# Optimization experiments

Measured on AMD Instinct MI355X. Metric: run time of the kernel, lower is better.

The kernel has to match this reference:

```python
import jax, jax.numpy as jnp
import numpy as np

D_MODEL = 1024
MAX_NUM_LAYERS = 4


def setup_inputs() -> dict:
    key = jax.random.key(0)
    ks = jax.random.split(key, 8)
    S, B, D, L = 1024, 2, D_MODEL, 3
    w = lambda k: (jax.random.normal(k, (D, D), dtype=jnp.float32) * 0.02)
    return {
        "x": jax.random.normal(ks[0], (S, B, D), dtype=jnp.float32),
        "layer_outputs": jax.random.normal(ks[1], (L, S, B, D), dtype=jnp.float32),
        "Wq": w(ks[2]), "bq": jnp.zeros((D,), jnp.float32),
        "Wk": w(ks[3]), "bk": jnp.zeros((D,), jnp.float32),
        "Wv": w(ks[4]), "bv": jnp.zeros((D,), jnp.float32),
        "Wo": w(ks[5]), "bo": jnp.zeros((D,), jnp.float32),
        "layer_weights": jnp.ones((MAX_NUM_LAYERS + 1,), jnp.float32),
        "num_heads": 16,
    }


def reference(x, layer_outputs, Wq, bq, Wk, bk, Wv, bv, Wo, bo, layer_weights, num_heads):
    # x: [S, B, D]; layer_outputs: [L, S, B, D] (stacked prev layer outputs)
    S, B, D = x.shape
    H = num_heads
    hd = D // H
    scale = hd ** -0.5
    # q from x only: [S, B*H, hd] -> [BH, S, hd]
    q = (x @ Wq.T + bq).reshape(S, B * H, hd).transpose(1, 0, 2)
    # k/v from x and all previous layer outputs (shared K/V projections)
    xs = jnp.concatenate([x[None], layer_outputs], axis=0)          # [Lp1, S, B, D]
    Lp1 = xs.shape[0]
    k = (xs @ Wk.T + bk).reshape(Lp1, S, B * H, hd).transpose(0, 2, 1, 3)  # [Lp1, BH, S, hd]
    v = (xs @ Wv.T + bv).reshape(Lp1, S, B * H, hd).transpose(0, 2, 1, 3)
    # per-layer scores, softmax over the key axis (torch dim=-2 of stacked scores)
    scores = jnp.einsum('bqd,lbkd->lbqk', q, k) * scale             # [Lp1, BH, S, S]
    attn = jax.nn.softmax(scores, axis=-1)
    lw = jax.nn.softmax(layer_weights[:Lp1])                        # [Lp1]
    combined = jnp.einsum('l,lbqk,lbkd->bqd', lw, attn, v)          # [BH, S, hd]
    combined = combined.transpose(1, 0, 2).reshape(S, B, D)
    return combined @ Wo.T + bo
```

## Files before the change

### kernel.cpp

```cpp
#include <hip/hip_runtime.h>
#include <hip/hip_bf16.h>
#include <math.h>

#define S_LEN   1024
#define BATCH   2
#define DMODEL  1024
#define NHEADS  16
#define HDIM    64
#define BHEADS  32
#define LP1     4
#define ROWS_PL 2048

typedef __attribute__((ext_vector_type(8)))  short bf16x8;
typedef __attribute__((ext_vector_type(4)))  float f32x4;
typedef __attribute__((ext_vector_type(16))) float f32x16;

__device__ inline ushort bf16_rne(float a) {
    unsigned u = __float_as_uint(a);
    return (ushort)((u + 0x7FFFu + ((u >> 16) & 1u)) >> 16);
}
__device__ inline float bf16_up(ushort h) { return __uint_as_float(((unsigned)h) << 16); }
__device__ inline void split_bf16(float a, ushort &hi, ushort &lo) {
    hi = bf16_rne(a);
    lo = bf16_rne(a - bf16_up(hi));
}
__device__ inline uint pk_bf16(float a, float b) {
    float2 f; f.x = a; f.y = b;
    __hip_bfloat162 h = __float22bfloat162_rn(f);
    return *reinterpret_cast<uint*>(&h);
}
#if __has_builtin(__builtin_amdgcn_exp2f)
__device__ inline float fast_exp2(float x) { return __builtin_amdgcn_exp2f(x); }
#else
__device__ inline float fast_exp2(float x) { return exp2f(x); }
#endif

__device__ inline void glds16(const ushort* g, ushort* l) {
    __builtin_amdgcn_global_load_lds(
        (const __attribute__((address_space(1))) void*)g,
        (__attribute__((address_space(3))) void*)l, 16, 0, 0);
}

#define SCLF 0.18033688011112042f

__global__ __launch_bounds__(256)
void presplit(const float* __restrict__ x, const float* __restrict__ lo,
              const float* __restrict__ Wq, const float* __restrict__ Wk,
              const float* __restrict__ Wv, const float* __restrict__ Wo,
              ushort* __restrict__ XsH, ushort* __restrict__ WH,
              ushort* __restrict__ WL)
{
    const int z = blockIdx.z;
    const float* src; ushort* dh; ushort* dl = nullptr; int n;
    if (z == 0)      { src = x;  dh = XsH;           n = 2097152; }
    else if (z == 1) { src = lo; dh = XsH + 2097152; n = 6291456; }
    else {
        const float* wsrc[4] = { Wq, Wk, Wv, Wo };
        src = wsrc[z - 2];
        dh = WH + (size_t)(z - 2) * 1048576;
        if (z == 2 || z == 5) dl = WL + (size_t)(z - 2) * 1048576;
        n = 1048576;
    }
    const int i = (blockIdx.x * 256 + threadIdx.x) * 8;
    if (i >= n) return;
    float v[8];
    *(float4*)&v[0] = *(const float4*)(src + i);
    *(float4*)&v[4] = *(const float4*)(src + i + 4);
    ushort h[8];
    #pragma unroll
    for (int j = 0; j < 8; ++j) h[j] = bf16_rne(v[j]);
    *(uint4*)(dh + i) = *(uint4*)h;
    if (dl) {
        ushort l[8];
        #pragma unroll
        for (int j = 0; j < 8; ++j) l[j] = bf16_rne(v[j] - bf16_up(h[j]));
        *(uint4*)(dl + i) = *(uint4*)l;
    }
}

template<int MODE>
__global__ __launch_bounds__(256)
void proj_g(const ushort* __restrict__ Abf,
            const ushort* __restrict__ Bhg, const ushort* __restrict__ Blg,
            const float* __restrict__ bias,
            float* __restrict__ outf, ushort* __restrict__ outh,
            ushort* __restrict__ outl)
{
    __shared__ ushort smem[3 * 2048];
    ushort* Ah = smem;
    ushort* Bh = smem + 2048;
    ushort* Bl = smem + 4096;

    const int fid = blockIdx.x;
    const int nt = (fid & 7) * 2 + ((fid >> 3) & 1);
    const int mt = fid >> 4;
    const int m0 = mt * 64, n0 = nt * 64;

    const int t  = threadIdx.x;
    const int wv = t >> 6, lane = t & 63;
    const int quad = lane >> 4, r = lane & 15;
    const int wm = wv & 1, wn = wv >> 1;
    const int mBase = wm * 32, nBase = wn * 32;

    const int lrow = lane >> 2;
    const int lch  = ((lane & 3) ^ (lrow & 3)) * 8;
    const ushort* Asrc  = Abf + (size_t)(m0 + wv * 16 + lrow) * DMODEL + lch;
    const ushort* Bhsrc = Bhg + (size_t)(n0 + wv * 16 + lrow) * DMODEL + lch;
    const ushort* Blsrc = Blg + (size_t)(n0 + wv * 16 + lrow) * DMODEL + lch;
    ushort* lA  = Ah + wv * 512;
    ushort* lBh = Bh + wv * 512;
    ushort* lBl = Bl + wv * 512;

    const int q0x = (quad ^ (r & 3)) << 3;
    f32x4 acc[2][2];
    #pragma unroll
    for (int i = 0; i < 2; ++i)
        #pragma unroll
        for (int j = 0; j < 2; ++j) acc[i][j] = (f32x4){0.f, 0.f, 0.f, 0.f};

    for (int k0 = 0; k0 < DMODEL; k0 += 32) {
        glds16(Asrc + k0, lA);
        glds16(Bhsrc + k0, lBh);
        glds16(Blsrc + k0, lBl);
        __syncthreads();
        bf16x8 fa[2], fbh[2], fbl[2];
        #pragma unroll
        for (int i = 0; i < 2; ++i)
            fa[i] = *(const bf16x8*)&Ah[(mBase + i * 16 + r) * 32 + q0x];
        #pragma unroll
        for (int j = 0; j < 2; ++j) {
            fbh[j] = *(const bf16x8*)&Bh[(nBase + j * 16 + r) * 32 + q0x];
            fbl[j] = *(const bf16x8*)&Bl[(nBase + j * 16 + r) * 32 + q0x];
        }
        #pragma unroll
        for (int i = 0; i < 2; ++i)
            #pragma unroll
            for (int j = 0; j < 2; ++j) {
                acc[i][j] = __builtin_amdgcn_mfma_f32_16x16x32_bf16(fa[i], fbh[j], acc[i][j], 0, 0, 0);
                acc[i][j] = __builtin_amdgcn_mfma_f32_16x16x32_bf16(fa[i], fbl[j], acc[i][j], 0, 0, 0);
            }
        __syncthreads();
    }

    const int cn = lane & 15;
    #pragma unroll
    for (int j = 0; j < 2; ++j) {
        const int n = n0 + nBase + j * 16 + cn;
        const float bv = bias[n];
        #pragma unroll
        for (int i = 0; i < 2; ++i) {
            const int mrow = m0 + mBase + i * 16 + quad * 4;
            #pragma unroll
            for (int g = 0; g < 4; ++g) {
                const int m = mrow + g;
                if (MODE == 1) {
                    outf[(size_t)m * DMODEL + n] = acc[i][j][g] + bv;
                } else {
                    const float val = (acc[i][j][g] + bv) * SCLF;
                    const int s = m >> 1, b = m & 1;
                    const int bh = b * 16 + (n >> 6), e = n & 63;
                    const size_t idx = (((size_t)bh * S_LEN) + s) * HDIM + e;
                    ushort hi, lov; split_bf16(val, hi, lov);
                    outh[idx] = hi; outl[idx] = lov;
                }
            }
        }
    }
}

__global__ __launch_bounds__(256, 4)
void proj_kv(const ushort* __restrict__ XsH,
             const ushort* __restrict__ KWh, const ushort* __restrict__ VWh,
             const float* __restrict__ bk, const float* __restrict__ bv,
             ushort* __restrict__ kout, ushort* __restrict__ vout)
{
    __shared__ ushort smem[10240];
    ushort* Ah = smem;
    ushort* Bp = smem + 2048;

    const int t  = threadIdx.x;
    const int m0 = blockIdx.y * 64, n0 = blockIdx.x * 128;
    const int lyr = m0 >> 11;

    const int wv = t >> 6, lane = t & 63;
    const int quad = lane >> 4, r = lane & 15;
    const int wm = wv & 1, wn = wv >> 1;
    const int mBase = wm * 32, nBase = wn * 64;

    const int lrow = lane >> 2;
    const int lch  = ((lane & 3) ^ (lrow & 3)) * 8;

    const ushort* Asrc = XsH + (size_t)(m0 + wv * 16 + lrow) * DMODEL + lch;
    const ushort* Bw[2] = { KWh, VWh };
    const ushort* Bsrc[2][2];
    #pragma unroll
    for (int p = 0; p < 2; ++p)
        #pragma unroll
        for (int seg = 0; seg < 2; ++seg)
            Bsrc[p][seg] = Bw[p] + (size_t)(n0 + wv * 32 + seg * 16 + lrow) * DMODEL + lch;

    const int q0x = (quad ^ (r & 3)) << 3;

    f32x4 aK[2][4], aV[2][4];
    #pragma unroll
    for (int i = 0; i < 2; ++i)
        #pragma unroll
        for (int j = 0; j < 4; ++j) {
            aK[i][j] = (f32x4){0.f, 0.f, 0.f, 0.f};
            aV[i][j] = (f32x4){0.f, 0.f, 0.f, 0.f};
        }

    for (int k0 = 0; k0 < DMODEL; k0 += 32) {
        glds16(Asrc + k0, Ah + wv * 512);
        #pragma unroll
        for (int p = 0; p < 2; ++p)
            #pragma unroll
            for (int seg = 0; seg < 2; ++seg)
                glds16(Bsrc[p][seg] + k0, Bp + p * 4096 + (wv * 2 + seg) * 512);
        __syncthreads();

        bf16x8 fa[2];
        #pragma unroll
        for (int i = 0; i < 2; ++i)
            fa[i] = *(const bf16x8*)&Ah[(mBase + i * 16 + r) * 32 + q0x];
        #pragma unroll
        for (int j = 0; j < 4; ++j) {
            const int off = (nBase + j * 16 + r) * 32 + q0x;
            const bf16x8 fkh = *(const bf16x8*)&Bp[off];
            const bf16x8 fvh = *(const bf16x8*)&Bp[4096 + off];
            #pragma unroll
            for (int i = 0; i < 2; ++i) {
                aK[i][j] = __builtin_amdgcn_mfma_f32_16x16x32_bf16(fa[i], fkh, aK[i][j], 0, 0, 0);
                aV[i][j] = __builtin_amdgcn_mfma_f32_16x16x32_bf16(fa[i], fvh, aV[i][j], 0, 0, 0);
            }
        }
        __syncthreads();
    }

    const int cn = lane & 15;

    #pragma unroll
    for (int j = 0; j < 4; ++j) {
        const int n = n0 + nBase + j * 16 + cn;
        const float bb = bk[n];
        #pragma unroll
        for (int i = 0; i < 2; ++i) {
            #pragma unroll
            for (int g = 0; g < 4; ++g) {
                const int m = m0 + mBase + i * 16 + quad * 4 + g;
                const int rem = m & 2047, s = rem >> 1, b = rem & 1;
                const int bh = lyr * 32 + b * 16 + (n >> 6);
                kout[(((size_t)bh * S_LEN) + s) * HDIM + (n & 63)] = bf16_rne(aK[i][j][g] + bb);
            }
        }
    }

    ushort* T = smem;
    __syncthreads();
    #pragma unroll
    for (int j = 0; j < 4; ++j) {
        const int nloc = nBase + j * 16 + cn;
        const float bb = bv[n0 + nloc];
        #pragma unroll
        for (int i = 0; i < 2; ++i) {
            #pragma unroll
            for (int g = 0; g < 4; ++g) {
                const int mloc = mBase + i * 16 + quad * 4 + g;
                T[nloc * 66 + mloc] = bf16_rne(aV[i][j][g] + bb);
            }
        }
    }
    __syncthreads();
    {
        const int nloc = t >> 1, bsel = t & 1;
        const int n = n0 + nloc, h = n >> 6, e = n & 63;
        const int s0g = (m0 & 2047) >> 1;
        const int bhI = lyr * 32 + bsel * 16 + h;
        ushort* dst = vout + ((size_t)bhI * HDIM + e) * S_LEN + s0g;
        #pragma unroll
        for (int c = 0; c < 4; ++c) {
            ushort tmp[8];
            #pragma unroll
            for (int j = 0; j < 8; ++j)
                tmp[j] = T[nloc * 66 + 2 * (c * 8 + j) + bsel];
            *(uint4*)(dst + c * 8) = *(uint4*)tmp;
        }
    }
}

__global__ __launch_bounds__(256, 2)
void attn_mfma(const ushort* __restrict__ qhg, const ushort* __restrict__ qlg,
               const ushort* __restrict__ kh, const ushort* __restrict__ vth,
               const float* __restrict__ lwraw, float* __restrict__ part)
{
    __shared__ ushort Pa[8 * 1280];

    const int t    = threadIdx.x;
    const int wv   = t >> 6, lane = t & 63;
    const int half = lane >> 5, lid = lane & 31;

    const int fid  = blockIdx.x;
    const int xcd  = fid & 7, slot = fid >> 3;
    const int pair = xcd * 16 + (slot >> 2);
    const int qt   = slot & 3;
    const int bh   = pair & 31, l = pair >> 5;
    const int qbase = qt * 256 + wv * 64;

    float wl;
    {
        float v[LP1], wm = -3.0e38f;
        #pragma unroll
        for (int i = 0; i < LP1; ++i) { v[i] = lwraw[i]; wm = fmaxf(wm, v[i]); }
        float ws = 0.f;
        #pragma unroll
        for (int i = 0; i < LP1; ++i) { v[i] = __expf(v[i] - wm); ws += v[i]; }
        wl = v[l] / ws;
    }

    bf16x8 qh[2][4], ql[2][4];
    #pragma unroll
    for (int u = 0; u < 2; ++u) {
        const size_t qoff = ((size_t)bh * S_LEN + qbase + u * 32 + lid) * HDIM + half * 8;
        #pragma unroll
        for (int es = 0; es < 4; ++es) {
            qh[u][es] = *(const bf16x8*)(qhg + qoff + es * 16);
            ql[u][es] = *(const bf16x8*)(qlg + qoff + es * 16);
        }
    }

    f32x16 o[2][2];
    #pragma unroll
    for (int u = 0; u < 2; ++u)
        #pragma unroll
        for (int d = 0; d < 2; ++d)
            #pragma unroll
            for (int i = 0; i < 16; ++i) o[u][d][i] = 0.f;
    float ls[2][16];
    #pragma unroll
    for (int u = 0; u < 2; ++u)
        #pragma unroll
        for (int i = 0; i < 16; ++i) ls[u][i] = 0.f;

    const size_t kvo = (size_t)(l * BHEADS + bh) * S_LEN * HDIM;

    for (int kt = 0; kt < 16; ++kt) {
        #pragma unroll
        for (int kc = 0; kc < 2; ++kc) {
            bf16x8 kb[4];
            #pragma unroll
            for (int es = 0; es < 4; ++es)
                kb[es] = *(const bf16x8*)(kh + kvo
                          + (size_t)(kt * 64 + kc * 32 + lid) * HDIM + es * 16 + half * 8);

            f32x16 sa[2];
            #pragma unroll
            for (int u = 0; u < 2; ++u)
                #pragma unroll
                for (int i = 0; i < 16; ++i) sa[u][i] = 0.f;
            #pragma unroll
            for (int es = 0; es < 4; ++es)
                #pragma unroll
                for (int u = 0; u < 2; ++u) {
                    sa[u] = __builtin_amdgcn_mfma_f32_32x32x16_bf16(qh[u][es], kb[es], sa[u], 0, 0, 0);
                    sa[u] = __builtin_amdgcn_mfma_f32_32x32x16_bf16(ql[u][es], kb[es], sa[u], 0, 0, 0);
                }

            bf16x8 vb[2][2];
            #pragma unroll
            for (int ks = 0; ks < 2; ++ks)
                #pragma unroll
                for (int dg = 0; dg < 2; ++dg)
                    vb[ks][dg] = *(const bf16x8*)(vth + kvo
                                  + (size_t)(dg * 32 + lid) * S_LEN
                                  + kt * 64 + kc * 32 + ks * 16 + half * 8);

            #pragma unroll
            for (int u = 0; u < 2; ++u) {
                ushort* base = &Pa[(wv * 2 + u) * 1280];
                #pragma unroll
                for (int rr = 0; rr < 16; rr += 2) {
                    const float p0 = fast_exp2(sa[u][rr]);
                    const float p1 = fast_exp2(sa[u][rr + 1]);
                    ls[u][rr]     += p0;
                    ls[u][rr + 1] += p1;
                    const uint pb = pk_bf16(p0, p1);
                    const int q0 = (rr & 3) + 8 * (rr >> 2) + 4 * half;
                    base[q0 * 40 + lid]       = (ushort)pb;
                    base[(q0 + 1) * 40 + lid] = (ushort)(pb >> 16);
                }
            }

            #pragma unroll
            for (int ks = 0; ks < 2; ++ks)
                #pragma unroll
                for (int u = 0; u < 2; ++u) {
                    const bf16x8 pf = *(const bf16x8*)
                        &Pa[(wv * 2 + u) * 1280 + lid * 40 + ks * 16 + half * 8];
                    #pragma unroll
                    for (int dg = 0; dg < 2; ++dg)
                        o[u][dg] = __builtin_amdgcn_mfma_f32_32x32x16_bf16(pf, vb[ks][dg], o[u][dg], 0, 0, 0);
                }
        }
    }

    #pragma unroll
    for (int u = 0; u < 2; ++u)
        #pragma unroll
        for (int rr = 0; rr < 16; ++rr) {
            float v = ls[u][rr];
            #pragma unroll
            for (int off = 1; off < 32; off <<= 1) v += __shfl_xor(v, off, 32);
            ls[u][rr] = v;
        }

    const int b = bh >> 4, hh = bh & 15;
    float* pbase = part + (size_t)l * (ROWS_PL * DMODEL);
    #pragma unroll
    for (int u = 0; u < 2; ++u)
        #pragma unroll
        for (int rr = 0; rr < 16; ++rr) {
            const int q = qbase + u * 32 + 8 * (rr >> 2) + 4 * half + (rr & 3);
            const float sc = wl / ls[u][rr];
            #pragma unroll
            for (int dg = 0; dg < 2; ++dg) {
                const int d = hh * HDIM + dg * 32 + lid;
                pbase[((size_t)q * BATCH + b) * DMODEL + d] = o[u][dg][rr] * sc;
            }
        }
}

__global__ __launch_bounds__(256)
void sum_y(const float* __restrict__ part, ushort* __restrict__ YH)
{
    const int i = (blockIdx.x * 256 + threadIdx.x) * 8;
    float acc[8];
    #pragma unroll
    for (int c = 0; c < 2; ++c) {
        float4 s = *(const float4*)(part + i + c * 4);
        #pragma unroll
        for (int l = 1; l < LP1; ++l) {
            const float4 p = *(const float4*)(part + (size_t)l * 2097152 + i + c * 4);
            s.x += p.x; s.y += p.y; s.z += p.z; s.w += p.w;
        }
        acc[c * 4 + 0] = s.x; acc[c * 4 + 1] = s.y;
        acc[c * 4 + 2] = s.z; acc[c * 4 + 3] = s.w;
    }
    uint out[4];
    #pragma unroll
    for (int c = 0; c < 4; ++c) out[c] = pk_bf16(acc[c * 2], acc[c * 2 + 1]);
    *(uint4*)(YH + i) = *(uint4*)out;
}

extern "C" void kernel_launch(void* const* d_in, const int* in_sizes, int n_in,
                              void* d_out, int out_size, void* d_ws, size_t ws_size,
                              hipStream_t stream) {
    const float* x  = (const float*)d_in[0];
    const float* lo = (const float*)d_in[1];
    const float* Wq = (const float*)d_in[2];
    const float* bq = (const float*)d_in[3];
    const float* Wk = (const float*)d_in[4];
    const float* bk = (const float*)d_in[5];
    const float* Wv = (const float*)d_in[6];
    const float* bv = (const float*)d_in[7];
    const float* Wo = (const float*)d_in[8];
    const float* bo = (const float*)d_in[9];
    const float* lw = (const float*)d_in[10];
    float* out = (float*)d_out;

    char* ws = (char*)d_ws;
    ushort* XsH  = (ushort*)(ws);
    ushort* WH   = (ushort*)(ws + 16777216);
    ushort* WL   = (ushort*)(ws + 25165824);
    ushort* qhb  = (ushort*)(ws + 33554432);
    ushort* qlb  = (ushort*)(ws + 37748736);
    ushort* khb  = (ushort*)(ws + 41943040);
    ushort* vthb = (ushort*)(ws + 58720256);
    float*  part = (float*)(ws + 75497472);
    ushort* YH   = (ushort*)(ws + 109051904);

    dim3 blk(256);
    presplit<<<dim3(3072, 1, 6), blk, 0, stream>>>(x, lo, Wq, Wk, Wv, Wo, XsH, WH, WL);
    proj_g<0><<<dim3(512), blk, 0, stream>>>(XsH, WH, WL, bq, nullptr, qhb, qlb);
    proj_kv<<<dim3(8, 128), blk, 0, stream>>>(XsH,
        WH + 1048576, WH + 2097152, bk, bv, khb, vthb);
    attn_mfma<<<dim3(512), blk, 0, stream>>>(qhb, qlb, khb, vthb, lw, part);
    sum_y<<<dim3(1024), blk, 0, stream>>>(part, YH);
    proj_g<1><<<dim3(512), blk, 0, stream>>>(YH, WH + 3145728, WL + 3145728, bo, out, nullptr, nullptr);
}
```

Measured before the change: 276.0 us.

## Transpose attention MFMA operands and pass P through permlane swap instead of LDS

The attention kernel now computes S^T = K·Q^T so each lane holds one query's scores. The P fragment for the PV MFMA is built in registers with v_permlane32_swap, which removes the LDS staging buffer and its stores and loads. Each wave now handles 32 queries instead of 64, the grid doubles to 1024 blocks, and launch bounds rise to 4 blocks per SIMD for more occupancy. The row-sum reduction collapses to a single cross-half shuffle, and output stores become float4. In exchange, K and V fragments are reused across half as many queries, so global/L2 load traffic per FLOP doubles.

```diff
diff --git a/kernel.cpp b/kernel.cpp
--- a/kernel.cpp
+++ b/kernel.cpp
@@ -34,6 +34,10 @@
 #else
 __device__ inline float fast_exp2(float x) { return exp2f(x); }
 #endif
+
+__device__ inline void permswap(uint &a, uint &b) {
+    asm("v_permlane32_swap_b32 %0, %1" : "+v"(a), "+v"(b));
+}
 
 __device__ inline void glds16(const ushort* g, ushort* l) {
     __builtin_amdgcn_global_load_lds(
@@ -288,23 +292,21 @@
     }
 }
 
-__global__ __launch_bounds__(256, 2)
+__global__ __launch_bounds__(256, 4)
 void attn_mfma(const ushort* __restrict__ qhg, const ushort* __restrict__ qlg,
                const ushort* __restrict__ kh, const ushort* __restrict__ vth,
                const float* __restrict__ lwraw, float* __restrict__ part)
 {
-    __shared__ ushort Pa[8 * 1280];
-
     const int t    = threadIdx.x;
     const int wv   = t >> 6, lane = t & 63;
     const int half = lane >> 5, lid = lane & 31;
 
     const int fid  = blockIdx.x;
     const int xcd  = fid & 7, slot = fid >> 3;
-    const int pair = xcd * 16 + (slot >> 2);
-    const int qt   = slot & 3;
+    const int pair = xcd * 16 + (slot >> 3);
+    const int qt   = slot & 7;
     const int bh   = pair & 31, l = pair >> 5;
-    const int qbase = qt * 256 + wv * 64;
+    const int qbase = qt * 128 + wv * 32;
 
     float wl;
     {
@@ -317,115 +319,87 @@
         wl = v[l] / ws;
     }
 
-    bf16x8 qh[2][4], ql[2][4];
-    #pragma unroll
-    for (int u = 0; u < 2; ++u) {
-        const size_t qoff = ((size_t)bh * S_LEN + qbase + u * 32 + lid) * HDIM + half * 8;
+    bf16x8 qh[4], ql[4];
+    {
+        const size_t qoff = ((size_t)bh * S_LEN + qbase + lid) * HDIM + half * 8;
         #pragma unroll
         for (int es = 0; es < 4; ++es) {
-            qh[u][es] = *(const bf16x8*)(qhg + qoff + es * 16);
-            ql[u][es] = *(const bf16x8*)(qlg + qoff + es * 16);
-        }
-    }
-
-    f32x16 o[2][2];
-    #pragma unroll
-    for (int u = 0; u < 2; ++u)
-        #pragma unroll
-        for (int d = 0; d < 2; ++d)
-            #pragma unroll
-            for (int i = 0; i < 16; ++i) o[u][d][i] = 0.f;
-    float ls[2][16];
-    #pragma unroll
-    for (int u = 0; u < 2; ++u)
-        #pragma unroll
-        for (int i = 0; i < 16; ++i) ls[u][i] = 0.f;
+            qh[es] = *(const bf16x8*)(qhg + qoff + es * 16);
+            ql[es] = *(const bf16x8*)(qlg + qoff + es * 16);
+        }
+    }
+
+    f32x16 o[2];
+    #pragma unroll
+    for (int dg = 0; dg < 2; ++dg)
+        #pragma unroll
+        for (int i = 0; i < 16; ++i) o[dg][i] = 0.f;
+    float ls = 0.f;
 
     const size_t kvo = (size_t)(l * BHEADS + bh) * S_LEN * HDIM;
 
-    for (int kt = 0; kt < 16; ++kt) {
-        #pragma unroll
-        for (int kc = 0; kc < 2; ++kc) {
-            bf16x8 kb[4];
-            #pragma unroll
-            for (int es = 0; es < 4; ++es)
-                kb[es] = *(const bf16x8*)(kh + kvo
-                          + (size_t)(kt * 64 + kc * 32 + lid) * HDIM + es * 16 + half * 8);
-
-            f32x16 sa[2];
-            #pragma unroll
-            for (int u = 0; u < 2; ++u)
-                #pragma unroll
-                for (int i = 0; i < 16; ++i) sa[u][i] = 0.f;
-            #pragma unroll
-            for (int es = 0; es < 4; ++es)
-                #pragma unroll
-                for (int u = 0; u < 2; ++u) {
-                    sa[u] = __builtin_amdgcn_mfma_f32_32x32x16_bf16(qh[u][es], kb[es], sa[u], 0, 0, 0);
-                    sa[u] = __builtin_amdgcn_mfma_f32_32x32x16_bf16(ql[u][es], kb[es], sa[u], 0, 0, 0);
-                }
-
-            bf16x8 vb[2][2];
-            #pragma unroll
-            for (int ks = 0; ks < 2; ++ks)
-                #pragma unroll
-                for (int dg = 0; dg < 2; ++dg)
-                    vb[ks][dg] = *(const bf16x8*)(vth + kvo
-                                  + (size_t)(dg * 32 + lid) * S_LEN
-                                  + kt * 64 + kc * 32 + ks * 16 + half * 8);
-
-            #pragma unroll
-            for (int u = 0; u < 2; ++u) {
-                ushort* base = &Pa[(wv * 2 + u) * 1280];
-                #pragma unroll
-                for (int rr = 0; rr < 16; rr += 2) {
-                    const float p0 = fast_exp2(sa[u][rr]);
-                    const float p1 = fast_exp2(sa[u][rr + 1]);
-                    ls[u][rr]     += p0;
-                    ls[u][rr + 1] += p1;
-                    const uint pb = pk_bf16(p0, p1);
-                    const int q0 = (rr & 3) + 8 * (rr >> 2) + 4 * half;
-                    base[q0 * 40 + lid]       = (ushort)pb;
-                    base[(q0 + 1) * 40 + lid] = (ushort)(pb >> 16);
-                }
-            }
-
-            #pragma unroll
-            for (int ks = 0; ks < 2; ++ks)
-                #pragma unroll
-                for (int u = 0; u < 2; ++u) {
-                    const bf16x8 pf = *(const bf16x8*)
-                        &Pa[(wv * 2 + u) * 1280 + lid * 40 + ks * 16 + half * 8];
-                    #pragma unroll
-                    for (int dg = 0; dg < 2; ++dg)
-                        o[u][dg] = __builtin_amdgcn_mfma_f32_32x32x16_bf16(pf, vb[ks][dg], o[u][dg], 0, 0, 0);
-                }
-        }
-    }
-
-    #pragma unroll
-    for (int u = 0; u < 2; ++u)
-        #pragma unroll
-        for (int rr = 0; rr < 16; ++rr) {
-            float v = ls[u][rr];
-            #pragma unroll
-            for (int off = 1; off < 32; off <<= 1) v += __shfl_xor(v, off, 32);
-            ls[u][rr] = v;
-        }
-
+    for (int kt = 0; kt < 32; ++kt) {
+        const ushort* kp = kh + kvo + (size_t)(kt * 32 + lid) * HDIM + half * 8;
+        bf16x8 kb[4];
+        #pragma unroll
+        for (int es = 0; es < 4; ++es) kb[es] = *(const bf16x8*)(kp + es * 16);
+
+        f32x16 sa;
+        #pragma unroll
+        for (int i = 0; i < 16; ++i) sa[i] = 0.f;
+        #pragma unroll
+        for (int es = 0; es < 4; ++es) {
+            sa = __builtin_amdgcn_mfma_f32_32x32x16_bf16(kb[es], qh[es], sa, 0, 0, 0);
+            sa = __builtin_amdgcn_mfma_f32_32x32x16_bf16(kb[es], ql[es], sa, 0, 0, 0);
+        }
+
+        const ushort* vp = vth + kvo + (size_t)lid * S_LEN + kt * 32 + half * 8;
+        #pragma unroll
+        for (int ks = 0; ks < 2; ++ks) {
+            const float p0 = fast_exp2(sa[8 * ks + 0]);
+            const float p1 = fast_exp2(sa[8 * ks + 1]);
+            const float p2 = fast_exp2(sa[8 * ks + 2]);
+            const float p3 = fast_exp2(sa[8 * ks + 3]);
+            const float p4 = fast_exp2(sa[8 * ks + 4]);
+            const float p5 = fast_exp2(sa[8 * ks + 5]);
+            const float p6 = fast_exp2(sa[8 * ks + 6]);
+            const float p7 = fast_exp2(sa[8 * ks + 7]);
+            ls += ((p0 + p1) + (p2 + p3)) + ((p4 + p5) + (p6 + p7));
+
+            uint a0 = pk_bf16(p0, p1);
+            uint a1 = pk_bf16(p2, p3);
+            uint b0 = pk_bf16(p4, p5);
+            uint b1 = pk_bf16(p6, p7);
+            permswap(a0, b0);
+            permswap(a1, b1);
+            union { uint w[4]; bf16x8 v; } pu;
+            pu.w[0] = a0; pu.w[1] = a1; pu.w[2] = b0; pu.w[3] = b1;
+            const bf16x8 pf = pu.v;
+
+            #pragma unroll
+            for (int dg = 0; dg < 2; ++dg) {
+                const bf16x8 vbf = *(const bf16x8*)(vp + (size_t)dg * (32 * S_LEN) + ks * 16);
+                o[dg] = __builtin_amdgcn_mfma_f32_32x32x16_bf16(vbf, pf, o[dg], 0, 0, 0);
+            }
+        }
+    }
+
+    ls += __shfl_xor(ls, 32);
+    const float sc = wl / ls;
     const int b = bh >> 4, hh = bh & 15;
-    float* pbase = part + (size_t)l * (ROWS_PL * DMODEL);
-    #pragma unroll
-    for (int u = 0; u < 2; ++u)
-        #pragma unroll
-        for (int rr = 0; rr < 16; ++rr) {
-            const int q = qbase + u * 32 + 8 * (rr >> 2) + 4 * half + (rr & 3);
-            const float sc = wl / ls[u][rr];
-            #pragma unroll
-            for (int dg = 0; dg < 2; ++dg) {
-                const int d = hh * HDIM + dg * 32 + lid;
-                pbase[((size_t)q * BATCH + b) * DMODEL + d] = o[u][dg][rr] * sc;
-            }
+    const int q = qbase + lid;
+    float* pb = part + (size_t)l * (ROWS_PL * DMODEL)
+              + ((size_t)q * BATCH + b) * DMODEL + hh * HDIM;
+    #pragma unroll
+    for (int dg = 0; dg < 2; ++dg)
+        #pragma unroll
+        for (int rq = 0; rq < 4; ++rq) {
+            float4 vv;
+            vv.x = o[dg][rq * 4 + 0] * sc;
+            vv.y = o[dg][rq * 4 + 1] * sc;
+            vv.z = o[dg][rq * 4 + 2] * sc;
+            vv.w = o[dg][rq * 4 + 3] * sc;
+            *(float4*)(pb + dg * 32 + rq * 8 + half * 4) = vv;
         }
 }
 
@@ -483,7 +457,7 @@
     proj_g<0><<<dim3(512), blk, 0, stream>>>(XsH, WH, WL, bq, nullptr, qhb, qlb);
     proj_kv<<<dim3(8, 128), blk, 0, stream>>>(XsH,
         WH + 1048576, WH + 2097152, bk, bv, khb, vthb);
-    attn_mfma<<<dim3(512), blk, 0, stream>>>(qhb, qlb, khb, vthb, lw, part);
+    attn_mfma<<<dim3(1024), blk, 0, stream>>>(qhb, qlb, khb, vthb, lw, part);
     sum_y<<<dim3(1024), blk, 0, stream>>>(part, YH);
     proj_g<1><<<dim3(512), blk, 0, stream>>>(YH, WH + 3145728, WL + 3145728, bo, out, nullptr, nullptr);
 }
```

Measured after the change: 328.5 us. 19.0% more time.

## Transpose attention MFMAs to keep softmax probabilities in registers via permlane swap

Applied to the files above, without the earlier changes.

The attention kernel now computes S^T (K as the A operand, Q as B), so each lane holds one query's scores along the key axis. A v_permlane32_swap repacks the bf16 probabilities directly into the B-operand layout of the PV MFMA, which removes the LDS round-trip for P. It also shrinks the row-sum bookkeeping to one scalar per tile, software-prefetches the next K tile into registers, raises wave priority around the MFMA blocks, and writes output with float4 stores. The new operand mapping and the inline asm must match the MFMA lane layout exactly, and the added prefetch registers may raise register pressure.

```diff
diff --git a/kernel.cpp b/kernel.cpp
--- a/kernel.cpp
+++ b/kernel.cpp
@@ -34,6 +34,10 @@
 #else
 __device__ inline float fast_exp2(float x) { return exp2f(x); }
 #endif
+
+__device__ inline void permswap(uint &a, uint &b) {
+    asm("v_permlane32_swap_b32 %0, %1" : "+v"(a), "+v"(b));
+}
 
 __device__ inline void glds16(const ushort* g, ushort* l) {
     __builtin_amdgcn_global_load_lds(
@@ -293,8 +297,6 @@
                const ushort* __restrict__ kh, const ushort* __restrict__ vth,
                const float* __restrict__ lwraw, float* __restrict__ part)
 {
-    __shared__ ushort Pa[8 * 1280];
-
     const int t    = threadIdx.x;
     const int wv   = t >> 6, lane = t & 63;
     const int half = lane >> 5, lid = lane & 31;
@@ -332,101 +334,114 @@
     #pragma unroll
     for (int u = 0; u < 2; ++u)
         #pragma unroll
-        for (int d = 0; d < 2; ++d)
-            #pragma unroll
-            for (int i = 0; i < 16; ++i) o[u][d][i] = 0.f;
-    float ls[2][16];
-    #pragma unroll
-    for (int u = 0; u < 2; ++u)
-        #pragma unroll
-        for (int i = 0; i < 16; ++i) ls[u][i] = 0.f;
+        for (int dg = 0; dg < 2; ++dg)
+            #pragma unroll
+            for (int i = 0; i < 16; ++i) o[u][dg][i] = 0.f;
+    float ls[2] = {0.f, 0.f};
 
     const size_t kvo = (size_t)(l * BHEADS + bh) * S_LEN * HDIM;
-
-    for (int kt = 0; kt < 16; ++kt) {
-        #pragma unroll
-        for (int kc = 0; kc < 2; ++kc) {
-            bf16x8 kb[4];
-            #pragma unroll
-            for (int es = 0; es < 4; ++es)
-                kb[es] = *(const bf16x8*)(kh + kvo
-                          + (size_t)(kt * 64 + kc * 32 + lid) * HDIM + es * 16 + half * 8);
-
-            f32x16 sa[2];
-            #pragma unroll
-            for (int u = 0; u < 2; ++u)
-                #pragma unroll
-                for (int i = 0; i < 16; ++i) sa[u][i] = 0.f;
-            #pragma unroll
-            for (int es = 0; es < 4; ++es)
-                #pragma unroll
-                for (int u = 0; u < 2; ++u) {
-                    sa[u] = __builtin_amdgcn_mfma_f32_32x32x16_bf16(qh[u][es], kb[es], sa[u], 0, 0, 0);
-                    sa[u] = __builtin_amdgcn_mfma_f32_32x32x16_bf16(ql[u][es], kb[es], sa[u], 0, 0, 0);
-                }
-
-            bf16x8 vb[2][2];
+    const ushort* kbase = kh + kvo + (size_t)lid * HDIM + half * 8;
+    const ushort* vbase = vth + kvo + (size_t)lid * S_LEN + half * 8;
+
+    bf16x8 kb[4];
+    #pragma unroll
+    for (int es = 0; es < 4; ++es)
+        kb[es] = *(const bf16x8*)(kbase + es * 16);
+
+    for (int kt = 0; kt < 32; ++kt) {
+        const int ktn = (kt + 1) & 31;
+        bf16x8 kn[4];
+        {
+            const ushort* kp = kbase + (size_t)ktn * 32 * HDIM;
+            #pragma unroll
+            for (int es = 0; es < 4; ++es) kn[es] = *(const bf16x8*)(kp + es * 16);
+        }
+        bf16x8 vb[2][2];
+        {
+            const ushort* vp = vbase + kt * 32;
             #pragma unroll
             for (int ks = 0; ks < 2; ++ks)
                 #pragma unroll
                 for (int dg = 0; dg < 2; ++dg)
-                    vb[ks][dg] = *(const bf16x8*)(vth + kvo
-                                  + (size_t)(dg * 32 + lid) * S_LEN
-                                  + kt * 64 + kc * 32 + ks * 16 + half * 8);
-
+                    vb[ks][dg] = *(const bf16x8*)(vp + (size_t)dg * (32 * S_LEN) + ks * 16);
+        }
+
+        f32x16 sa[2];
+        #pragma unroll
+        for (int u = 0; u < 2; ++u)
+            #pragma unroll
+            for (int i = 0; i < 16; ++i) sa[u][i] = 0.f;
+
+        __builtin_amdgcn_s_setprio(1);
+        #pragma unroll
+        for (int es = 0; es < 4; ++es)
             #pragma unroll
             for (int u = 0; u < 2; ++u) {
-                ushort* base = &Pa[(wv * 2 + u) * 1280];
+                sa[u] = __builtin_amdgcn_mfma_f32_32x32x16_bf16(kb[es], qh[u][es], sa[u], 0, 0, 0);
+                sa[u] = __builtin_amdgcn_mfma_f32_32x32x16_bf16(kb[es], ql[u][es], sa[u], 0, 0, 0);
+            }
+        __builtin_amdgcn_s_setprio(0);
+
+        #pragma unroll
+        for (int ks = 0; ks < 2; ++ks) {
+            bf16x8 pf[2];
+            #pragma unroll
+            for (int u = 0; u < 2; ++u) {
+                const float p0 = fast_exp2(sa[u][8 * ks + 0]);
+                const float p1 = fast_exp2(sa[u][8 * ks + 1]);
+                const float p2 = fast_exp2(sa[u][8 * ks + 2]);
+                const float p3 = fast_exp2(sa[u][8 * ks + 3]);
+                const float p4 = fast_exp2(sa[u][8 * ks + 4]);
+                const float p5 = fast_exp2(sa[u][8 * ks + 5]);
+                const float p6 = fast_exp2(sa[u][8 * ks + 6]);
+                const float p7 = fast_exp2(sa[u][8 * ks + 7]);
+                ls[u] += ((p0 + p1) + (p2 + p3)) + ((p4 + p5) + (p6 + p7));
+
+                uint a0 = pk_bf16(p0, p1);
+                uint a1 = pk_bf16(p2, p3);
+                uint b0 = pk_bf16(p4, p5);
+                uint b1 = pk_bf16(p6, p7);
+                permswap(a0, b0);
+                permswap(a1, b1);
+                union { uint w[4]; bf16x8 v; } pu;
+                pu.w[0] = a0; pu.w[1] = a1; pu.w[2] = b0; pu.w[3] = b1;
+                pf[u] = pu.v;
+            }
+
+            __builtin_amdgcn_s_setprio(1);
+            #pragma unroll
+            for (int dg = 0; dg < 2; ++dg)
                 #pragma unroll
-                for (int rr = 0; rr < 16; rr += 2) {
-                    const float p0 = fast_exp2(sa[u][rr]);
-                    const float p1 = fast_exp2(sa[u][rr + 1]);
-                    ls[u][rr]     += p0;
-                    ls[u][rr + 1] += p1;
-                    const uint pb = pk_bf16(p0, p1);
-                    const int q0 = (rr & 3) + 8 * (rr >> 2) + 4 * half;
-                    base[q0 * 40 + lid]       = (ushort)pb;
-                    base[(q0 + 1) * 40 + lid] = (ushort)(pb >> 16);
-                }
-            }
-
-            #pragma unroll
-            for (int ks = 0; ks < 2; ++ks)
-                #pragma unroll
-                for (int u = 0; u < 2; ++u) {
-                    const bf16x8 pf = *(const bf16x8*)
-                        &Pa[(wv * 2 + u) * 1280 + lid * 40 + ks * 16 + half * 8];
-                    #pragma unroll
-                    for (int dg = 0; dg < 2; ++dg)
-                        o[u][dg] = __builtin_amdgcn_mfma_f32_32x32x16_bf16(pf, vb[ks][dg], o[u][dg], 0, 0, 0);
-                }
-        }
-    }
-
-    #pragma unroll
-    for (int u = 0; u < 2; ++u)
-        #pragma unroll
-        for (int rr = 0; rr < 16; ++rr) {
-            float v = ls[u][rr];
-            #pragma unroll
-            for (int off = 1; off < 32; off <<= 1) v += __shfl_xor(v, off, 32);
-            ls[u][rr] = v;
-        }
+                for (int u = 0; u < 2; ++u)
+                    o[u][dg] = __builtin_amdgcn_mfma_f32_32x32x16_bf16(vb[ks][dg], pf[u], o[u][dg], 0, 0, 0);
+            __builtin_amdgcn_s_setprio(0);
+        }
+
+        #pragma unroll
+        for (int es = 0; es < 4; ++es) kb[es] = kn[es];
+    }
 
     const int b = bh >> 4, hh = bh & 15;
-    float* pbase = part + (size_t)l * (ROWS_PL * DMODEL);
-    #pragma unroll
-    for (int u = 0; u < 2; ++u)
-        #pragma unroll
-        for (int rr = 0; rr < 16; ++rr) {
-            const int q = qbase + u * 32 + 8 * (rr >> 2) + 4 * half + (rr & 3);
-            const float sc = wl / ls[u][rr];
-            #pragma unroll
-            for (int dg = 0; dg < 2; ++dg) {
-                const int d = hh * HDIM + dg * 32 + lid;
-                pbase[((size_t)q * BATCH + b) * DMODEL + d] = o[u][dg][rr] * sc;
-            }
-        }
+    #pragma unroll
+    for (int u = 0; u < 2; ++u) {
+        float lsv = ls[u];
+        lsv += __shfl_xor(lsv, 32);
+        const float sc = wl / lsv;
+        const int q = qbase + u * 32 + lid;
+        float* pb = part + (size_t)l * (ROWS_PL * DMODEL)
+                  + ((size_t)q * BATCH + b) * DMODEL + hh * HDIM;
+        #pragma unroll
+        for (int dg = 0; dg < 2; ++dg)
+            #pragma unroll
+            for (int rq = 0; rq < 4; ++rq) {
+                float4 vv;
+                vv.x = o[u][dg][rq * 4 + 0] * sc;
+                vv.y = o[u][dg][rq * 4 + 1] * sc;
+                vv.z = o[u][dg][rq * 4 + 2] * sc;
+                vv.w = o[u][dg][rq * 4 + 3] * sc;
+                *(float4*)(pb + dg * 32 + rq * 8 + half * 4) = vv;
+            }
+    }
 }
 
 __global__ __launch_bounds__(256)
```

After: 273.3 us. No clear change (-1.0%).
